# Performance work log

Measured on AMD Instinct MI355X. Metric: run time of the kernel, lower is better.

## Reference

```python
import jax, jax.numpy as jnp
import numpy as np

EPS = 1e-5  # torch BatchNorm1d default eps

# BinActive: sign forward, straight-through estimator backward (grad clipped where |x|>1)
@jax.custom_vjp
def bin_active(x):
    return jnp.sign(x)

def _ba_fwd(x):
    return jnp.sign(x), x

def _ba_bwd(x, g):
    return (g * (jnp.abs(x) <= 1.0).astype(g.dtype),)

bin_active.defvjp(_ba_fwd, _ba_bwd)

# XNOR-style weight binarization: sign(W) * mean(|W|) per output column, STE backward
@jax.custom_vjp
def bin_weight(w):
    alpha = jnp.mean(jnp.abs(w), axis=0, keepdims=True)  # [1, out]
    return jnp.sign(w) * alpha

def _bw_fwd(w):
    alpha = jnp.mean(jnp.abs(w), axis=0, keepdims=True)
    return jnp.sign(w) * alpha, w

def _bw_bwd(w, g):
    return (g * (jnp.abs(w) <= 1.0).astype(g.dtype),)

bin_weight.defvjp(_bw_fwd, _bw_bwd)


def setup_inputs() -> dict:
    key = jax.random.key(0)
    ks = jax.random.split(key, 8)
    N, E, IN, H, OUT = 100000, 1600000, 256, 128, 40
    x = jax.random.normal(ks[0], (N, IN), dtype=jnp.float32)
    edge_index = jax.random.randint(ks[1], (2, E), 0, N, dtype=jnp.int64)
    W0 = jax.random.normal(ks[2], (IN, H), dtype=jnp.float32) * (2.0 / IN) ** 0.5
    b0 = jnp.zeros((H,), dtype=jnp.float32)
    W1 = jax.random.normal(ks[3], (H, H), dtype=jnp.float32) * (2.0 / H) ** 0.5
    b1 = jnp.zeros((H,), dtype=jnp.float32)
    W2 = jax.random.normal(ks[4], (H, OUT), dtype=jnp.float32) * (2.0 / H) ** 0.5
    b2 = jnp.zeros((OUT,), dtype=jnp.float32)
    return {"x": x, "edge_index": edge_index, "W0": W0, "b0": b0,
            "W1": W1, "b1": b1, "W2": W2, "b2": b2}


def reference(x, edge_index, W0, b0, W1, b1, W2, b2):
    n = x.shape[0]
    loop = jnp.arange(n, dtype=edge_index.dtype)
    src = jnp.concatenate([edge_index[0], loop])  # add self loops (GCN norm)
    dst = jnp.concatenate([edge_index[1], loop])
    deg = jax.ops.segment_sum(jnp.ones_like(src, dtype=x.dtype), dst, num_segments=n)
    dinv = jnp.where(deg > 0, deg ** -0.5, 0.0)
    norm = (dinv[src] * dinv[dst])[:, None]  # [E+N, 1]

    # BatchNorm1d(affine=False), training-mode batch statistics (biased var)
    mu = jnp.mean(x, axis=0)
    var = jnp.var(x, axis=0)
    h = (x - mu) * jax.lax.rsqrt(var + EPS)

    for W, b in ((W0, b0), (W1, b1), (W2, b2)):
        h = bin_active(h)                       # sign binarize (dropout skipped: eval)
        h = h @ bin_weight(W)                   # binary-weight linear
        h = jax.ops.segment_sum(h[src] * norm, dst, num_segments=n) + b  # D^-1/2 (A+I) D^-1/2 agg
    return jax.nn.log_softmax(h, axis=1)
```

## Files before the change

kernel.cpp:

```cpp
#include <hip/hip_runtime.h>
#include <math.h>

#define IN_DIM 256
#define HD 128
#define OUT_DIM 40
#define S2_STRIDE 64
#define NB_CS 512

__global__ __launch_bounds__(256) void k_init(int* deg, float* muacc, int N) {
    int i = blockIdx.x * 256 + threadIdx.x;
    if (i < N) deg[i] = 1;
    if (blockIdx.x == 0 && threadIdx.x < 256) muacc[threadIdx.x] = 0.f;
}

__global__ __launch_bounds__(256) void k_fuse1(const float* __restrict__ x, int N,
                                               float* __restrict__ muacc,
                                               const int* __restrict__ ei, int E, int* deg,
                                               int* __restrict__ rank, int ebl,
                                               const float* __restrict__ W0,
                                               const float* __restrict__ W1,
                                               const float* __restrict__ W2,
                                               unsigned long long* W0p,
                                               unsigned long long* W1p,
                                               unsigned long long* W2p,
                                               float* aS0, float* aS1, float* aS2) {
    __shared__ float lds[256];
    int b = blockIdx.x, tid = threadIdx.x;
    if (b < NB_CS) {
        size_t F4 = (size_t)N * (IN_DIM / 4);
        size_t stride = (size_t)NB_CS * 256;
        float a0 = 0.f, a1 = 0.f, a2 = 0.f, a3 = 0.f;
        const float4* x4 = (const float4*)x;
        for (size_t i = (size_t)b * 256 + tid; i < F4; i += stride) {
            float4 v = x4[i];
            a0 += v.x; a1 += v.y; a2 += v.z; a3 += v.w;
        }
        lds[tid] = 0.f;
        __syncthreads();
        int c0 = (tid * 4) & 255;
        atomicAdd(&lds[c0], a0);
        atomicAdd(&lds[c0 + 1], a1);
        atomicAdd(&lds[c0 + 2], a2);
        atomicAdd(&lds[c0 + 3], a3);
        __syncthreads();
        atomicAdd(&muacc[tid], lds[tid]);
    } else if (b < NB_CS + ebl) {
        int e = (b - NB_CS) * 256 + tid;
        if (e < E) {
            int old = atomicAdd(&deg[ei[E + e]], 1);
            rank[e] = old - 1;
        }
    } else {
        int b2 = b - NB_CS - ebl;
        int lane = tid & 63, w = tid >> 6;
        if (b2 < 32) {
            int j = b2 * 4 + w;
            float asum = 0.f;
            unsigned long long words[4];
            #pragma unroll
            for (int q = 0; q < 4; ++q) {
                float v = W0[(size_t)(4 * lane + q) * HD + j];
                asum += fabsf(v);
                words[q] = __ballot(v < 0.f);
            }
            #pragma unroll
            for (int off = 32; off; off >>= 1) asum += __shfl_xor(asum, off);
            if (lane == 0) {
                aS0[j] = 2.f * asum / 256.f;
                #pragma unroll
                for (int q = 0; q < 4; ++q) W0p[j * 4 + q] = words[q];
            }
        } else if (b2 < 64) {
            int j = (b2 - 32) * 4 + w;
            int fl = lane & 15, kk = lane >> 4;
            float asum = 0.f;
            unsigned long long words[2];
            #pragma unroll
            for (int q = 0; q < 2; ++q) {
                float v = W1[(size_t)(fl * 8 + 4 * q + kk) * HD + j];
                asum += fabsf(v);
                words[q] = __ballot(v < 0.f);
            }
            #pragma unroll
            for (int off = 32; off; off >>= 1) asum += __shfl_xor(asum, off);
            if (lane == 0) {
                aS1[j] = 2.f * asum / 128.f;
                W1p[j * 2 + 0] = words[0];
                W1p[j * 2 + 1] = words[1];
            }
        } else {
            int j = (b2 - 64) * 4 + w;
            int fl = lane & 15, kk = lane >> 4;
            if (j < OUT_DIM) {
                float asum = 0.f;
                unsigned long long words[2];
                #pragma unroll
                for (int q = 0; q < 2; ++q) {
                    float v = W2[(size_t)(fl * 8 + 4 * q + kk) * OUT_DIM + j];
                    asum += fabsf(v);
                    words[q] = __ballot(v < 0.f);
                }
                #pragma unroll
                for (int off = 32; off; off >>= 1) asum += __shfl_xor(asum, off);
                if (lane == 0) {
                    aS2[j] = 2.f * asum / 128.f;
                    W2p[j * 2 + 0] = words[0];
                    W2p[j * 2 + 1] = words[1];
                }
            }
        }
    }
}

__global__ __launch_bounds__(256) void k_bp(const int* __restrict__ deg, int N, int* bp) {
    __shared__ int sm[256];
    int i = blockIdx.x * 256 + threadIdx.x;
    sm[threadIdx.x] = (i < N) ? (deg[i] - 1) : 0;
    __syncthreads();
    for (int off = 128; off; off >>= 1) {
        if (threadIdx.x < off) sm[threadIdx.x] += sm[threadIdx.x + off];
        __syncthreads();
    }
    if (threadIdx.x == 0) bp[blockIdx.x] = sm[0];
}

__global__ __launch_bounds__(512) void k_scanbp(const int* __restrict__ bp, int NB, int* bps) {
    __shared__ int sm[512];
    int t = threadIdx.x;
    int v = (t < NB) ? bp[t] : 0;
    sm[t] = v;
    __syncthreads();
    for (int off = 1; off < 512; off <<= 1) {
        int add = (t >= off) ? sm[t - off] : 0;
        __syncthreads();
        sm[t] += add;
        __syncthreads();
    }
    if (t < NB) bps[t] = sm[t] - v;
}

__global__ __launch_bounds__(256) void k_rowptr(const int* __restrict__ deg,
                                                const int* __restrict__ bps, int N, int E,
                                                int* row_ptr, float* dinv) {
    __shared__ int wsum[4];
    int t = threadIdx.x, lane = t & 63, w = t >> 6;
    int i = blockIdx.x * 256 + t;
    int c = (i < N) ? (deg[i] - 1) : 0;
    int v = c;
    #pragma unroll
    for (int off = 1; off < 64; off <<= 1) {
        int n = __shfl_up(v, off);
        if (lane >= off) v += n;
    }
    if (lane == 63) wsum[w] = v;
    __syncthreads();
    int wo = 0;
    for (int k = 0; k < w; ++k) wo += wsum[k];
    int excl = bps[blockIdx.x] + wo + v - c;
    if (i < N) {
        row_ptr[i] = excl;
        dinv[i] = (float)(1.0 / sqrt((double)deg[i]));
    }
    if (blockIdx.x == 0 && t == 0) row_ptr[N] = E;
}

__global__ __launch_bounds__(256) void k_fuse2(const int* __restrict__ ei, int E,
                                               const float* __restrict__ dinv,
                                               const int* __restrict__ rowp,
                                               const int* __restrict__ rank,
                                               long long* __restrict__ cs, int nbScat,
                                               const float* __restrict__ x,
                                               const float* __restrict__ muacc, float inv_n,
                                               const unsigned long long* __restrict__ W0p,
                                               unsigned char* __restrict__ S0, int N) {
    __shared__ unsigned long long w0s[128 * 4];
    int b = blockIdx.x, tid = threadIdx.x;
    if (b < nbScat) {
        int e = b * 256 + tid;
        if (e >= E) return;
        int s = ei[e];
        int d = ei[E + e];
        int pos = rowp[d] + rank[e];
        float nrm = dinv[s] * dinv[d];
        long long v = (long long)(unsigned int)s |
                      ((long long)(unsigned int)__float_as_int(nrm) << 32);
        __builtin_nontemporal_store(v, &cs[pos]);
    } else {
        w0s[tid] = W0p[tid];
        w0s[tid + 256] = W0p[tid + 256];
        __syncthreads();
        int lane = tid & 63;
        int row = (b - nbScat) * 4 + (tid >> 6);
        if (row >= N) return;
        float4 xv = ((const float4*)(x + (size_t)row * IN_DIM))[lane];
        float4 ms = ((const float4*)muacc)[lane];
        unsigned long long xw[4];
        xw[0] = __ballot(xv.x < ms.x * inv_n);
        xw[1] = __ballot(xv.y < ms.y * inv_n);
        xw[2] = __ballot(xv.z < ms.z * inv_n);
        xw[3] = __ballot(xv.w < ms.w * inv_n);
        unsigned int pack = 0;
        #pragma unroll
        for (int t2 = 0; t2 < 2; ++t2) {
            int j = 2 * lane + t2;
            const unsigned long long* wc = &w0s[j * 4];
            int dd = __popcll(xw[0] ^ wc[0]) + __popcll(xw[1] ^ wc[1]) +
                     __popcll(xw[2] ^ wc[2]) + __popcll(xw[3] ^ wc[3]);
            int S = IN_DIM - 2 * dd;
            int s8 = S >> 1;
            if (s8 > 127) s8 = 127;
            pack |= ((unsigned int)(s8 + 128) & 0xffu) << (8 * t2);
        }
        *(unsigned short*)(S0 + (size_t)row * HD + 2 * lane) = (unsigned short)pack;
    }
}

template <int OUTC>
__global__ __launch_bounds__(256) void k_agg_mm(const unsigned char* __restrict__ Sin,
                                                const int* __restrict__ row_ptr,
                                                const long long* __restrict__ cs,
                                                const float* __restrict__ dinv,
                                                const float* __restrict__ alphaS,
                                                const float* __restrict__ bias,
                                                const unsigned long long* __restrict__ Wnp,
                                                unsigned char* __restrict__ Sout, int N) {
    __shared__ unsigned long long wsm[OUTC * 2];
    int tid = threadIdx.x;
    for (int i = tid; i < OUTC * 2; i += 256) wsm[i] = Wnp[i];
    __syncthreads();
    int lane = tid & 63;
    int d = blockIdx.x * 4 + (tid >> 6);
    if (d >= N) return;
    int sub = lane >> 4;
    int fl  = lane & 15;
    float acc[8];
    #pragma unroll
    for (int k = 0; k < 8; ++k) acc[k] = 0.f;
    if (sub == 0) {
        float dv = dinv[d];
        float nrm = dv * dv;
        unsigned long long r = *(const unsigned long long*)(Sin + (size_t)d * HD + fl * 8);
        unsigned int lo = (unsigned int)r, hi = (unsigned int)(r >> 32);
        #pragma unroll
        for (int k = 0; k < 4; ++k) {
            acc[k]     = fmaf(nrm, (float)((lo >> (8 * k)) & 0xffu) - 128.f, acc[k]);
            acc[k + 4] = fmaf(nrm, (float)((hi >> (8 * k)) & 0xffu) - 128.f, acc[k + 4]);
        }
    }
    int e0 = row_ptr[d], e1 = row_ptr[d + 1];
    int e = e0 + sub;
    for (; e + 4 < e1; e += 8) {
        long long pa = cs[e];
        long long pb = cs[e + 4];
        int sa = (int)(unsigned int)pa;
        int sb = (int)(unsigned int)pb;
        unsigned long long ra = *(const unsigned long long*)(Sin + (size_t)sa * HD + fl * 8);
        unsigned long long rb = *(const unsigned long long*)(Sin + (size_t)sb * HD + fl * 8);
        float na = __int_as_float((int)(pa >> 32));
        float nb = __int_as_float((int)(pb >> 32));
        unsigned int la = (unsigned int)ra, ha = (unsigned int)(ra >> 32);
        unsigned int lb = (unsigned int)rb, hb = (unsigned int)(rb >> 32);
        #pragma unroll
        for (int k = 0; k < 4; ++k) {
            acc[k]     = fmaf(na, (float)((la >> (8 * k)) & 0xffu) - 128.f, acc[k]);
            acc[k + 4] = fmaf(na, (float)((ha >> (8 * k)) & 0xffu) - 128.f, acc[k + 4]);
            acc[k]     = fmaf(nb, (float)((lb >> (8 * k)) & 0xffu) - 128.f, acc[k]);
            acc[k + 4] = fmaf(nb, (float)((hb >> (8 * k)) & 0xffu) - 128.f, acc[k + 4]);
        }
    }
    if (e < e1) {
        long long p = cs[e];
        int s = (int)(unsigned int)p;
        float nrm = __int_as_float((int)(p >> 32));
        unsigned long long r = *(const unsigned long long*)(Sin + (size_t)s * HD + fl * 8);
        unsigned int lo = (unsigned int)r, hi = (unsigned int)(r >> 32);
        #pragma unroll
        for (int k = 0; k < 4; ++k) {
            acc[k]     = fmaf(nrm, (float)((lo >> (8 * k)) & 0xffu) - 128.f, acc[k]);
            acc[k + 4] = fmaf(nrm, (float)((hi >> (8 * k)) & 0xffu) - 128.f, acc[k + 4]);
        }
    }
    #pragma unroll
    for (int k = 0; k < 8; ++k) {
        acc[k] += __shfl_xor(acc[k], 16);
        acc[k] += __shfl_xor(acc[k], 32);
    }
    unsigned int m8 = 0;
    #pragma unroll
    for (int k = 0; k < 8; ++k) {
        int f = fl * 8 + k;
        float v = alphaS[f] * acc[k] + bias[f];
        if (v < 0.f) m8 |= (1u << k);
    }
    unsigned long long x0 = 0, x1 = 0;
    #pragma unroll
    for (int k = 0; k < 4; ++k) {
        unsigned long long bk = __ballot((m8 >> k) & 1u);
        x0 |= (bk & 0xffffULL) << (16 * k);
    }
    #pragma unroll
    for (int k = 4; k < 8; ++k) {
        unsigned long long bk = __ballot((m8 >> k) & 1u);
        x1 |= (bk & 0xffffULL) << (16 * (k - 4));
    }
    if (OUTC == 128) {
        unsigned int pack = 0;
        #pragma unroll
        for (int t2 = 0; t2 < 2; ++t2) {
            int j = 2 * lane + t2;
            int dd = __popcll(x0 ^ wsm[j * 2]) + __popcll(x1 ^ wsm[j * 2 + 1]);
            int S = HD - 2 * dd;
            pack |= ((unsigned int)((S >> 1) + 128) & 0xffu) << (8 * t2);
        }
        *(unsigned short*)(Sout + (size_t)d * HD + 2 * lane) = (unsigned short)pack;
    } else {
        int p8 = 128;
        if (lane < OUTC) {
            int dd = __popcll(x0 ^ wsm[lane * 2]) + __popcll(x1 ^ wsm[lane * 2 + 1]);
            p8 = ((HD - 2 * dd) >> 1) + 128;
        }
        Sout[(size_t)d * S2_STRIDE + lane] = (unsigned char)p8;
    }
}

__global__ __launch_bounds__(256) void k_agg_out(const unsigned char* __restrict__ S2,
                                                 const int* __restrict__ row_ptr,
                                                 const long long* __restrict__ cs,
                                                 const float* __restrict__ dinv,
                                                 const float* __restrict__ alphaS2,
                                                 const float* __restrict__ b2,
                                                 float* __restrict__ out, int N) {
    int tid = threadIdx.x, lane = tid & 63;
    int d = blockIdx.x * 4 + (tid >> 6);
    if (d >= N) return;
    int sub = lane >> 4;
    int fl  = lane & 15;
    float acc[4] = {0.f, 0.f, 0.f, 0.f};
    if (sub == 0) {
        float dv = dinv[d];
        float nrm = dv * dv;
        unsigned int r4 = *(const unsigned int*)(S2 + (size_t)d * S2_STRIDE + fl * 4);
        #pragma unroll
        for (int k = 0; k < 4; ++k)
            acc[k] = fmaf(nrm, (float)((r4 >> (8 * k)) & 0xffu) - 128.f, acc[k]);
    }
    int e0 = row_ptr[d], e1 = row_ptr[d + 1];
    int e = e0 + sub;
    for (; e + 4 < e1; e += 8) {
        long long pa = cs[e];
        long long pb = cs[e + 4];
        int sa = (int)(unsigned int)pa;
        int sb = (int)(unsigned int)pb;
        unsigned int ra = *(const unsigned int*)(S2 + (size_t)sa * S2_STRIDE + fl * 4);
        unsigned int rb = *(const unsigned int*)(S2 + (size_t)sb * S2_STRIDE + fl * 4);
        float na = __int_as_float((int)(pa >> 32));
        float nb = __int_as_float((int)(pb >> 32));
        #pragma unroll
        for (int k = 0; k < 4; ++k) {
            acc[k] = fmaf(na, (float)((ra >> (8 * k)) & 0xffu) - 128.f, acc[k]);
            acc[k] = fmaf(nb, (float)((rb >> (8 * k)) & 0xffu) - 128.f, acc[k]);
        }
    }
    if (e < e1) {
        long long p = cs[e];
        int s = (int)(unsigned int)p;
        float nrm = __int_as_float((int)(p >> 32));
        unsigned int r4 = *(const unsigned int*)(S2 + (size_t)s * S2_STRIDE + fl * 4);
        #pragma unroll
        for (int k = 0; k < 4; ++k)
            acc[k] = fmaf(nrm, (float)((r4 >> (8 * k)) & 0xffu) - 128.f, acc[k]);
    }
    #pragma unroll
    for (int k = 0; k < 4; ++k) {
        acc[k] += __shfl_xor(acc[k], 16);
        acc[k] += __shfl_xor(acc[k], 32);
    }
    float h[4];
    float mymax = -INFINITY;
    #pragma unroll
    for (int k = 0; k < 4; ++k) {
        int f = fl * 4 + k;
        h[k] = (f < OUT_DIM) ? (alphaS2[f] * acc[k] + b2[f]) : -INFINITY;
        mymax = fmaxf(mymax, h[k]);
    }
    #pragma unroll
    for (int off = 1; off < 16; off <<= 1) mymax = fmaxf(mymax, __shfl_xor(mymax, off));
    float s4 = 0.f;
    #pragma unroll
    for (int k = 0; k < 4; ++k) {
        if (fl * 4 + k < OUT_DIM) s4 += expf(h[k] - mymax);
    }
    #pragma unroll
    for (int off = 1; off < 16; off <<= 1) s4 += __shfl_xor(s4, off);
    float lse = mymax + logf(s4);
    if (sub == 0 && fl < OUT_DIM / 4) {
        float4 o;
        o.x = h[0] - lse; o.y = h[1] - lse; o.z = h[2] - lse; o.w = h[3] - lse;
        *(float4*)(out + (size_t)d * OUT_DIM + fl * 4) = o;
    }
}

extern "C" void kernel_launch(void* const* d_in, const int* in_sizes, int n_in,
                              void* d_out, int out_size, void* d_ws, size_t ws_size,
                              hipStream_t stream) {
    const float* x  = (const float*)d_in[0];
    const int*   ei = (const int*)d_in[1];
    const float* W0 = (const float*)d_in[2];
    const float* b0 = (const float*)d_in[3];
    const float* W1 = (const float*)d_in[4];
    const float* b1 = (const float*)d_in[5];
    const float* W2 = (const float*)d_in[6];
    const float* b2 = (const float*)d_in[7];
    float* out = (float*)d_out;

    int N = in_sizes[0] / IN_DIM;
    int E = in_sizes[1] / 2;

    char* ws = (char*)d_ws;
    size_t off = 0;
    auto alloc = [&](size_t bytes) -> void* {
        off = (off + 255) & ~(size_t)255;
        void* p = (void*)(ws + off);
        off += bytes;
        return p;
    };
    float* muacc  = (float*)alloc(256 * 4);
    int*   deg    = (int*)alloc((size_t)N * 4);
    float* dinv   = (float*)alloc((size_t)N * 4);
    int*   rowp   = (int*)alloc(((size_t)N + 1) * 4);
    int*   bp     = (int*)alloc(512 * 4);
    int*   bps    = (int*)alloc(512 * 4);
    int*   rank   = (int*)alloc((size_t)E * 4);
    long long* cs = (long long*)alloc((size_t)E * 8);
    unsigned char* S0 = (unsigned char*)alloc((size_t)N * HD);
    unsigned char* S1 = (unsigned char*)alloc((size_t)N * HD);
    unsigned char* S2 = (unsigned char*)alloc((size_t)N * S2_STRIDE);
    unsigned long long* W0p = (unsigned long long*)alloc(128 * 4 * 8);
    unsigned long long* W1p = (unsigned long long*)alloc(128 * 2 * 8);
    unsigned long long* W2p = (unsigned long long*)alloc(40 * 2 * 8);
    float* aS0 = (float*)alloc(128 * 4);
    float* aS1 = (float*)alloc(128 * 4);
    float* aS2 = (float*)alloc(40 * 4);

    int nb256 = (N + 255) / 256;
    int ebl = (E + 255) / 256;
    float inv_n = 1.0f / (float)N;

    k_init<<<dim3(nb256), dim3(256), 0, stream>>>(deg, muacc, N);
    k_fuse1<<<dim3(NB_CS + ebl + 74), dim3(256), 0, stream>>>(
        x, N, muacc, ei, E, deg, rank, ebl, W0, W1, W2, W0p, W1p, W2p, aS0, aS1, aS2);
    k_bp<<<dim3(nb256), dim3(256), 0, stream>>>(deg, N, bp);
    k_scanbp<<<dim3(1), dim3(512), 0, stream>>>(bp, nb256, bps);
    k_rowptr<<<dim3(nb256), dim3(256), 0, stream>>>(deg, bps, N, E, rowp, dinv);

    int nb4 = (N + 3) / 4;
    k_fuse2<<<dim3(ebl + nb4), dim3(256), 0, stream>>>(
        ei, E, dinv, rowp, rank, cs, ebl, x, muacc, inv_n, W0p, S0, N);
    k_agg_mm<128><<<dim3(nb4), dim3(256), 0, stream>>>(S0, rowp, cs, dinv, aS0, b0, W1p, S1, N);
    k_agg_mm<40><<<dim3(nb4), dim3(256), 0, stream>>>(S1, rowp, cs, dinv, aS1, b1, W2p, S2, N);
    k_agg_out<<<dim3(nb4), dim3(256), 0, stream>>>(S2, rowp, cs, dinv, aS2, b2, out, N);
    (void)out_size; (void)ws_size; (void)n_in;
}
```

Baseline: 511.8 us.

## Privatize degree and mean atomics per XCD with workgroup-scope atomics

Degree counting and column-sum accumulation now use per-XCD private arrays, indexed by the hardware XCC id and updated with relaxed workgroup-scope atomics. The aim is to avoid cross-die coherent atomics going through the device-wide memory path. A later pass combines the per-XCD counts into per-node offsets, and the CSR scatter adds the XCD offset plus a local rank packed into the top bits of rank. The change also doubles the column-sum block count, and moves dinv computation and the mean reduction into existing small kernels. The cost is extra memory traffic for 8x-sized degree and offset arrays. Correctness now relies on all blocks of one XCD sharing an L2, so workgroup-scope atomics must stay coherent within that XCD.

```diff
diff --git a/kernel.cpp b/kernel.cpp
--- a/kernel.cpp
+++ b/kernel.cpp
@@ -5,17 +5,24 @@
 #define HD 128
 #define OUT_DIM 40
 #define S2_STRIDE 64
-#define NB_CS 512
-
-__global__ __launch_bounds__(256) void k_init(int* deg, float* muacc, int N) {
+#define NB_CS 1024
+#define NXCD 8
+
+__device__ __forceinline__ int xcc_id() {
+    int x;
+    asm volatile("s_getreg_b32 %0, hwreg(HW_REG_XCC_ID)" : "=s"(x));
+    return x & (NXCD - 1);
+}
+
+__global__ __launch_bounds__(256) void k_init(int* deg8, float* muacc8, int N8) {
     int i = blockIdx.x * 256 + threadIdx.x;
-    if (i < N) deg[i] = 1;
-    if (blockIdx.x == 0 && threadIdx.x < 256) muacc[threadIdx.x] = 0.f;
+    if (i < N8) deg8[i] = 0;
+    if (i < NXCD * 256) muacc8[i] = 0.f;
 }
 
 __global__ __launch_bounds__(256) void k_fuse1(const float* __restrict__ x, int N,
-                                               float* __restrict__ muacc,
-                                               const int* __restrict__ ei, int E, int* deg,
+                                               float* __restrict__ muacc8,
+                                               const int* __restrict__ ei, int E, int* deg8,
                                                int* __restrict__ rank, int ebl,
                                                const float* __restrict__ W0,
                                                const float* __restrict__ W1,
@@ -43,12 +50,17 @@
         atomicAdd(&lds[c0 + 2], a2);
         atomicAdd(&lds[c0 + 3], a3);
         __syncthreads();
-        atomicAdd(&muacc[tid], lds[tid]);
+        int xc = xcc_id();
+        __hip_atomic_fetch_add(&muacc8[xc * 256 + tid], lds[tid],
+                               __ATOMIC_RELAXED, __HIP_MEMORY_SCOPE_WORKGROUP);
     } else if (b < NB_CS + ebl) {
         int e = (b - NB_CS) * 256 + tid;
         if (e < E) {
-            int old = atomicAdd(&deg[ei[E + e]], 1);
-            rank[e] = old - 1;
+            int d = ei[E + e];
+            int xc = xcc_id();
+            int old = __hip_atomic_fetch_add(&deg8[(size_t)xc * N + d], 1,
+                                             __ATOMIC_RELAXED, __HIP_MEMORY_SCOPE_WORKGROUP);
+            rank[e] = old | (xc << 28);
         }
     } else {
         int b2 = b - NB_CS - ebl;
@@ -112,10 +124,25 @@
     }
 }
 
-__global__ __launch_bounds__(256) void k_bp(const int* __restrict__ deg, int N, int* bp) {
+__global__ __launch_bounds__(256) void k_bp(const int* __restrict__ deg8, int N, int* bp,
+                                            int* __restrict__ xoff, float* __restrict__ dinv,
+                                            int* __restrict__ cnt) {
     __shared__ int sm[256];
     int i = blockIdx.x * 256 + threadIdx.x;
-    sm[threadIdx.x] = (i < N) ? (deg[i] - 1) : 0;
+    int c = 0;
+    if (i < N) {
+        int run = 0;
+        #pragma unroll
+        for (int xc = 0; xc < NXCD; ++xc) {
+            int v = deg8[(size_t)xc * N + i];
+            xoff[(size_t)xc * N + i] = run;
+            run += v;
+        }
+        c = run;
+        cnt[i] = run;
+        dinv[i] = (float)(1.0 / sqrt((double)(run + 1)));
+    }
+    sm[threadIdx.x] = c;
     __syncthreads();
     for (int off = 128; off; off >>= 1) {
         if (threadIdx.x < off) sm[threadIdx.x] += sm[threadIdx.x + off];
@@ -124,9 +151,17 @@
     if (threadIdx.x == 0) bp[blockIdx.x] = sm[0];
 }
 
-__global__ __launch_bounds__(512) void k_scanbp(const int* __restrict__ bp, int NB, int* bps) {
+__global__ __launch_bounds__(512) void k_scanbp(const int* __restrict__ bp, int NB, int* bps,
+                                                const float* __restrict__ muacc8,
+                                                float* __restrict__ mu) {
     __shared__ int sm[512];
     int t = threadIdx.x;
+    if (t < 256) {
+        float s = 0.f;
+        #pragma unroll
+        for (int xc = 0; xc < NXCD; ++xc) s += muacc8[xc * 256 + t];
+        mu[t] = s;
+    }
     int v = (t < NB) ? bp[t] : 0;
     sm[t] = v;
     __syncthreads();
@@ -139,13 +174,13 @@
     if (t < NB) bps[t] = sm[t] - v;
 }
 
-__global__ __launch_bounds__(256) void k_rowptr(const int* __restrict__ deg,
+__global__ __launch_bounds__(256) void k_rowptr(const int* __restrict__ cnt,
                                                 const int* __restrict__ bps, int N, int E,
-                                                int* row_ptr, float* dinv) {
+                                                int* row_ptr) {
     __shared__ int wsum[4];
     int t = threadIdx.x, lane = t & 63, w = t >> 6;
     int i = blockIdx.x * 256 + t;
-    int c = (i < N) ? (deg[i] - 1) : 0;
+    int c = (i < N) ? cnt[i] : 0;
     int v = c;
     #pragma unroll
     for (int off = 1; off < 64; off <<= 1) {
@@ -157,10 +192,7 @@
     int wo = 0;
     for (int k = 0; k < w; ++k) wo += wsum[k];
     int excl = bps[blockIdx.x] + wo + v - c;
-    if (i < N) {
-        row_ptr[i] = excl;
-        dinv[i] = (float)(1.0 / sqrt((double)deg[i]));
-    }
+    if (i < N) row_ptr[i] = excl;
     if (blockIdx.x == 0 && t == 0) row_ptr[N] = E;
 }
 
@@ -168,6 +200,7 @@
                                                const float* __restrict__ dinv,
                                                const int* __restrict__ rowp,
                                                const int* __restrict__ rank,
+                                               const int* __restrict__ xoff,
                                                long long* __restrict__ cs, int nbScat,
                                                const float* __restrict__ x,
                                                const float* __restrict__ muacc, float inv_n,
@@ -180,7 +213,10 @@
         if (e >= E) return;
         int s = ei[e];
         int d = ei[E + e];
-        int pos = rowp[d] + rank[e];
+        int r = rank[e];
+        int xc = ((unsigned int)r) >> 28;
+        int lr = r & 0x0FFFFFFF;
+        int pos = rowp[d] + xoff[(size_t)xc * N + d] + lr;
         float nrm = dinv[s] * dinv[d];
         long long v = (long long)(unsigned int)s |
                       ((long long)(unsigned int)__float_as_int(nrm) << 32);
@@ -424,8 +460,11 @@
         off += bytes;
         return p;
     };
-    float* muacc  = (float*)alloc(256 * 4);
-    int*   deg    = (int*)alloc((size_t)N * 4);
+    float* mu     = (float*)alloc(256 * 4);
+    float* muacc8 = (float*)alloc(NXCD * 256 * 4);
+    int*   deg8   = (int*)alloc((size_t)NXCD * N * 4);
+    int*   xoff   = (int*)alloc((size_t)NXCD * N * 4);
+    int*   cnt    = (int*)alloc((size_t)N * 4);
     float* dinv   = (float*)alloc((size_t)N * 4);
     int*   rowp   = (int*)alloc(((size_t)N + 1) * 4);
     int*   bp     = (int*)alloc(512 * 4);
@@ -444,18 +483,20 @@
 
     int nb256 = (N + 255) / 256;
     int ebl = (E + 255) / 256;
+    int N8 = NXCD * N;
+    int nbInit = (N8 + 255) / 256;
     float inv_n = 1.0f / (float)N;
 
-    k_init<<<dim3(nb256), dim3(256), 0, stream>>>(deg, muacc, N);
+    k_init<<<dim3(nbInit), dim3(256), 0, stream>>>(deg8, muacc8, N8);
     k_fuse1<<<dim3(NB_CS + ebl + 74), dim3(256), 0, stream>>>(
-        x, N, muacc, ei, E, deg, rank, ebl, W0, W1, W2, W0p, W1p, W2p, aS0, aS1, aS2);
-    k_bp<<<dim3(nb256), dim3(256), 0, stream>>>(deg, N, bp);
-    k_scanbp<<<dim3(1), dim3(512), 0, stream>>>(bp, nb256, bps);
-    k_rowptr<<<dim3(nb256), dim3(256), 0, stream>>>(deg, bps, N, E, rowp, dinv);
+        x, N, muacc8, ei, E, deg8, rank, ebl, W0, W1, W2, W0p, W1p, W2p, aS0, aS1, aS2);
+    k_bp<<<dim3(nb256), dim3(256), 0, stream>>>(deg8, N, bp, xoff, dinv, cnt);
+    k_scanbp<<<dim3(1), dim3(512), 0, stream>>>(bp, nb256, bps, muacc8, mu);
+    k_rowptr<<<dim3(nb256), dim3(256), 0, stream>>>(cnt, bps, N, E, rowp);
 
     int nb4 = (N + 3) / 4;
     k_fuse2<<<dim3(ebl + nb4), dim3(256), 0, stream>>>(
-        ei, E, dinv, rowp, rank, cs, ebl, x, muacc, inv_n, W0p, S0, N);
+        ei, E, dinv, rowp, rank, xoff, cs, ebl, x, mu, inv_n, W0p, S0, N);
     k_agg_mm<128><<<dim3(nb4), dim3(256), 0, stream>>>(S0, rowp, cs, dinv, aS0, b0, W1p, S1, N);
     k_agg_mm<40><<<dim3(nb4), dim3(256), 0, stream>>>(S1, rowp, cs, dinv, aS1, b1, W2p, S2, N);
     k_agg_out<<<dim3(nb4), dim3(256), 0, stream>>>(S2, rowp, cs, dinv, aS2, b2, out, N);
```

Measured after the change: 497.9 us. 1.03x faster.
